# Kernel optimization log

Measured on AMD Instinct MI355X. Metric: run time of the kernel, lower is better.

## Reference

```python
import jax, jax.numpy as jnp
import numpy as np

NUM_IMUS = 13
NUM_PARAMS = 9
EPS = 1e-5
LN_EPS = 1e-5


def setup_inputs() -> dict:
    key = jax.random.key(0)
    k1, k2, k3 = jax.random.split(key, 3)
    d_model, S = 512, 2048
    hidden_states = jax.random.normal(k1, (1, S, d_model), dtype=jnp.float32)
    min_orig_accel_norm = jax.random.normal(k2, (1,), dtype=jnp.float32)
    W = jax.random.normal(k3, (d_model, NUM_IMUS * NUM_PARAMS), dtype=jnp.float32) * 0.02
    b = jnp.zeros((NUM_IMUS * NUM_PARAMS,), jnp.float32)
    ln_w = jnp.ones((d_model,), jnp.float32)
    ln_b = jnp.zeros((d_model,), jnp.float32)
    return {"hidden_states": hidden_states, "min_orig_accel_norm": min_orig_accel_norm,
            "ln_w": ln_w, "ln_b": ln_b, "W": W, "b": b}


def _layernorm(x, w, bias):
    mu = x.mean(-1, keepdims=True)
    var = ((x - mu) ** 2).mean(-1, keepdims=True)
    return (x - mu) * jax.lax.rsqrt(var + LN_EPS) * w + bias


def reference(hidden_states, min_orig_accel_norm, ln_w, ln_b, W, b):
    S = hidden_states.shape[1]
    x = _layernorm(hidden_states, ln_w, ln_b)
    # (1,S,117) -> (S, 9, 13); batch is always 1
    p = (x @ W + b).reshape(S, NUM_PARAMS, NUM_IMUS)
    c, c_th, phi, phi_th = p[:, 4], p[:, 5], p[:, 6], p[:, 7]  # (S,13) each
    d = jnp.sqrt(p[:, 1] ** 2 + EPS)                 # (S,13)
    k = d ** 2 / 4 + jax.nn.softplus(p[:, 0])
    d_th = jnp.sqrt(p[:, 3] ** 2 + EPS)
    k_th = d_th ** 2 / 4 + jax.nn.softplus(p[:, 2])
    noise_bias = p[:, 8].T                           # (13,S)
    om = jnp.sqrt(4 * k - d ** 2) / 2                # = sqrt(softplus(p0))
    om_th = jnp.sqrt(4 * k_th - d_th ** 2) / 2
    t = jnp.arange(S, dtype=jnp.float32)
    tstep = jnp.triu(t[None, :] - t[:, None])        # (S,S), entry (i,j)=j-i for j>=i
    ts = tstep[:, :, None]                           # (S,S,1)

    def src(a):  # params indexed by source step i, broadcast over target step j
        return a[:, None, :]                         # (S,1,13)

    lin = src(c) * jnp.exp(-src(d) / 2 * ts) * jnp.sin(ts * src(om) + src(phi))
    ang = src(c_th) * jnp.exp(-src(d_th) / 2 * ts) * jnp.sin(ts * src(om_th) + src(phi_th))
    mask = jnp.triu(jnp.ones((S, S), jnp.float32))[:, :, None]
    summed = ((lin + ang) * mask).sum(axis=0)        # (S,13): sum over source i<=j
    return summed.T + min_orig_accel_norm + noise_bias  # (13,S)
```

## Files before the change

### kernel.cpp

```cpp
#include <hip/hip_runtime.h>
#include <math.h>

#define S_LEN 2048
#define D_MODEL 512
#define NIMU 13
#define NCOL 117
#define CPAD 128
#define NKC 8
#define KCSTRIDE ((size_t)CPAD * S_LEN)

static __device__ __forceinline__ float softplus_f(float x) {
    return (x > 20.f) ? x : log1pf(expf(x));
}

static __device__ __forceinline__ void osc_init(float pk, float pd, float amp, float phi, float dtf,
                                                float& re, float& im, float& zr, float& zi)
{
    const float LOG2E = 1.4426950408889634f;
    const float INV2PI = 0.15915494309189535f;
    float d = sqrtf(pd * pd + 1e-5f);
    float kk = d * d * 0.25f + softplus_f(pk);
    float om = 0.5f * sqrtf(fmaxf(4.f * kk - d * d, 0.f));
    float y = -0.5f * d * LOG2E;
    float f = om * INV2PI;
    float ph = phi * INV2PI;
    float ez = __builtin_amdgcn_exp2f(y);
    zr = ez * __builtin_amdgcn_cosf(f);
    zi = ez * __builtin_amdgcn_sinf(f);
    float er = amp * __builtin_amdgcn_exp2f(dtf * y);
    float r = fmaf(dtf, f, ph); r -= floorf(r);
    re = er * __builtin_amdgcn_cosf(r);
    im = er * __builtin_amdgcn_sinf(r);
}

__global__ __launch_bounds__(256) void stats_kernel(const float* __restrict__ H,
                                                    float2* __restrict__ stats,
                                                    const float* __restrict__ W,
                                                    float* __restrict__ Wp,
                                                    float* __restrict__ out) {
    if (blockIdx.x < 104) out[blockIdx.x * 256 + threadIdx.x] = 0.f;
    if (threadIdx.x < CPAD) {
        int c = threadIdx.x;
        Wp[blockIdx.x * CPAD + c] = (c < NCOL) ? W[blockIdx.x * NCOL + c] : 0.f;
    }
    int wave = threadIdx.x >> 6;
    int lane = threadIdx.x & 63;
    int row = blockIdx.x * 4 + wave;
    const float* hr = H + row * D_MODEL;
    float4 a = *(const float4*)&hr[lane * 4];
    float4 b = *(const float4*)&hr[256 + lane * 4];
    float sum = a.x + a.y + a.z + a.w + b.x + b.y + b.z + b.w;
    #pragma unroll
    for (int off = 32; off; off >>= 1) sum += __shfl_down(sum, off);
    sum = __shfl(sum, 0);
    float mu = sum * (1.f / 512.f);
    float vs = 0.f;
    vs += (a.x - mu) * (a.x - mu); vs += (a.y - mu) * (a.y - mu);
    vs += (a.z - mu) * (a.z - mu); vs += (a.w - mu) * (a.w - mu);
    vs += (b.x - mu) * (b.x - mu); vs += (b.y - mu) * (b.y - mu);
    vs += (b.z - mu) * (b.z - mu); vs += (b.w - mu) * (b.w - mu);
    #pragma unroll
    for (int off = 32; off; off >>= 1) vs += __shfl_down(vs, off);
    if (lane == 0) {
        float var = vs * (1.f / 512.f);
        stats[row] = make_float2(mu, 1.0f / sqrtf(var + 1e-5f));
    }
}

__global__ __launch_bounds__(128) void proj_kernel(
    const float* __restrict__ H, const float2* __restrict__ stats,
    const float* __restrict__ lnw, const float* __restrict__ lnb,
    const float* __restrict__ Wp, float* __restrict__ Pt)
{
    __shared__ float Xt[64 * 32];
    __shared__ float Ws[64 * CPAD];
    int tid = threadIdx.x;
    int row0 = blockIdx.x * 32;
    int k0 = blockIdx.y * 64;

    {
        const float4* Wp4 = (const float4*)(Wp + k0 * CPAD);
        float4* Ws4 = (float4*)Ws;
        #pragma unroll
        for (int i = 0; i < 16; ++i) Ws4[tid + i * 128] = Wp4[tid + i * 128];
    }
    {
        int r = tid >> 2, fq = tid & 3;
        int row = row0 + r;
        float2 st = stats[row];
        const float4* H4 = (const float4*)(H + row * D_MODEL + k0);
        const float4* w4 = (const float4*)(lnw + k0);
        const float4* b4 = (const float4*)(lnb + k0);
        #pragma unroll
        for (int it = 0; it < 4; ++it) {
            int q = fq + it * 4;
            float4 h = H4[q], wv = w4[q], bv = b4[q];
            Xt[(4 * q + 0) * 32 + r] = (h.x - st.x) * st.y * wv.x + bv.x;
            Xt[(4 * q + 1) * 32 + r] = (h.y - st.x) * st.y * wv.y + bv.y;
            Xt[(4 * q + 2) * 32 + r] = (h.z - st.x) * st.y * wv.z + bv.z;
            Xt[(4 * q + 3) * 32 + r] = (h.w - st.x) * st.y * wv.w + bv.w;
        }
    }
    __syncthreads();

    int q8 = tid & 15;
    int rg = tid >> 4;
    float acc[4][8];
    #pragma unroll
    for (int a = 0; a < 4; ++a)
        for (int u = 0; u < 8; ++u) acc[a][u] = 0.f;

    #pragma unroll 4
    for (int k = 0; k < 64; ++k) {
        float4 xa = *(float4*)&Xt[k * 32 + 4 * rg];
        float4 w0 = *(float4*)&Ws[k * CPAD + 8 * q8];
        float4 w1 = *(float4*)&Ws[k * CPAD + 8 * q8 + 4];
        float xv[4] = {xa.x, xa.y, xa.z, xa.w};
        float wv[8] = {w0.x, w0.y, w0.z, w0.w, w1.x, w1.y, w1.z, w1.w};
        #pragma unroll
        for (int a = 0; a < 4; ++a)
            #pragma unroll
            for (int u = 0; u < 8; ++u)
                acc[a][u] = fmaf(xv[a], wv[u], acc[a][u]);
    }

    if (q8 < 15) {
        #pragma unroll
        for (int u = 0; u < 8; ++u) {
            int c = 8 * q8 + u;
            if (c < NCOL) {
                float4 v = make_float4(acc[0][u], acc[1][u], acc[2][u], acc[3][u]);
                *(float4*)&Pt[((size_t)blockIdx.y * CPAD + c) * S_LEN + row0 + 4 * rg] = v;
            }
        }
    }
}

__global__ __launch_bounds__(256) void reduce_kernel(const float* __restrict__ Pt,
                                                     const float* __restrict__ bias,
                                                     float* __restrict__ Pred)
{
    int c = blockIdx.y;
    int s4 = blockIdx.x * 256 + threadIdx.x;
    const float4* p4 = (const float4*)(Pt + (size_t)c * S_LEN) + s4;
    float b = bias[c];
    float4 acc = make_float4(b, b, b, b);
    #pragma unroll
    for (int kc = 0; kc < NKC; ++kc) {
        float4 v = p4[kc * (KCSTRIDE / 4)];
        acc.x += v.x; acc.y += v.y; acc.z += v.z; acc.w += v.w;
    }
    ((float4*)(Pred + (size_t)c * S_LEN))[s4] = acc;
}

__global__ __launch_bounds__(256) void main_kernel(
    const float* __restrict__ Pred,
    const float* __restrict__ minp, float* __restrict__ out)
{
    __shared__ float buf[4 * 128];
    int tid = threadIdx.x;
    int lane = tid & 63, w = tid >> 6;
    int m = blockIdx.y;
    int bx = blockIdx.x;

    int g = 0, base = 0;
    #pragma unroll 1
    for (;;) {
        int nb = (g + 4) >> 2;
        if (bx < base + nb) break;
        base += nb; ++g;
    }
    int sub = bx - base;
    int q = sub * 4 + w;

    float* accW = buf + w * 128;
    accW[lane] = 0.f; accW[lane + 64] = 0.f;
    __builtin_amdgcn_wave_barrier();

    if (q <= g) {
        int sc = q, tc = g - q;
        int i0 = sc * 64;
        float dtf = (float)(tc * 64);

        float pv[9];
        #pragma unroll
        for (int p = 0; p < 9; ++p)
            pv[p] = Pred[(size_t)(p * 13 + m) * S_LEN + i0 + lane];

        float reL, imL, zrL, ziL; osc_init(pv[0], pv[1], pv[4], pv[6], dtf, reL, imL, zrL, ziL);
        float reA, imA, zrA, ziA; osc_init(pv[2], pv[3], pv[5], pv[7], dtf, reA, imA, zrA, ziA);

        float a = 0.f;
        #pragma unroll 8
        for (int t = 0; t < 64; ++t) {
            a += imL + imA;
            accW[lane + t] = a;
            __builtin_amdgcn_wave_barrier();
            float nxt = accW[lane + t + 1];
            float tL = imL * ziL; float rL = fmaf(reL, zrL, -tL);
            imL = fmaf(reL, ziL, imL * zrL); reL = rL;
            float tA = imA * ziA; float rA = fmaf(reA, zrA, -tA);
            imA = fmaf(reA, ziA, imA * zrA); reA = rA;
            a = nxt;
        }
    }
    __syncthreads();

    if (tid < 128) {
        int j = g * 64 + tid;
        if (j < S_LEN) {
            float s = buf[tid] + buf[128 + tid] + buf[256 + tid] + buf[384 + tid];
            if (sub == 0 && tid < 64) {
                s += minp[0] + Pred[(size_t)(8 * 13 + m) * S_LEN + j];
            }
            atomicAdd(&out[m * S_LEN + j], s);
        }
    }
}

extern "C" void kernel_launch(void* const* d_in, const int* in_sizes, int n_in,
                              void* d_out, int out_size, void* d_ws, size_t ws_size,
                              hipStream_t stream)
{
    const float* H    = (const float*)d_in[0];
    const float* MINP = (const float*)d_in[1];
    const float* LNW  = (const float*)d_in[2];
    const float* LNB  = (const float*)d_in[3];
    const float* W    = (const float*)d_in[4];
    const float* B    = (const float*)d_in[5];
    float* out = (float*)d_out;

    const size_t PTSZ = (size_t)NKC * CPAD * S_LEN * sizeof(float);
    const size_t STSZ = S_LEN * sizeof(float2);
    const size_t WPSZ = (size_t)D_MODEL * CPAD * sizeof(float);

    char* ws = (char*)d_ws;
    float*  Pt    = (float*)ws;
    float2* stats = (float2*)(ws + PTSZ);
    float*  Wp    = (float*)(ws + PTSZ + STSZ);
    float*  Pred  = (float*)(ws + PTSZ + STSZ + WPSZ);

    stats_kernel<<<512, 256, 0, stream>>>(H, stats, W, Wp, out);
    proj_kernel<<<dim3(64, 8), 128, 0, stream>>>(H, stats, LNW, LNB, Wp, Pt);
    reduce_kernel<<<dim3(2, NCOL), 256, 0, stream>>>(Pt, B, Pred);
    main_kernel<<<dim3(144, NIMU), 256, 0, stream>>>(Pred, MINP, out);
}
```

Measured before the change: 92.04 us.

## Process two source steps per lane in main kernel to halve tile count

Each lane of the oscillator-sum kernel now handles two adjacent source steps, using 128-wide source chunks instead of 64. Both oscillators advance each step, and their contributions are interleaved through a 192-entry shared shift buffer per wave. This roughly halves the number of blocks (144 to 80 per IMU) and the per-step LDS shift traffic per source element, amortising the barrier and store/load costs. In exchange it uses more registers and a more complex indexing scheme with a wider 192-column output reduction.

After: 95.03 us. 1.03x slower.

```diff
diff --git a/kernel.cpp b/kernel.cpp
--- a/kernel.cpp
+++ b/kernel.cpp
@@ -157,7 +157,7 @@
     const float* __restrict__ Pred,
     const float* __restrict__ minp, float* __restrict__ out)
 {
-    __shared__ float buf[4 * 128];
+    __shared__ float buf[4 * 192];
     int tid = threadIdx.x;
     int lane = tid & 63, w = tid >> 6;
     int m = blockIdx.y;
@@ -166,50 +166,65 @@
     int g = 0, base = 0;
     #pragma unroll 1
     for (;;) {
-        int nb = (g + 4) >> 2;
+        int nb = ((g >> 1) + 4) >> 2;
         if (bx < base + nb) break;
         base += nb; ++g;
     }
     int sub = bx - base;
     int q = sub * 4 + w;
 
-    float* accW = buf + w * 128;
-    accW[lane] = 0.f; accW[lane + 64] = 0.f;
+    float* accW = buf + w * 192;
+    accW[lane] = 0.f; accW[lane + 64] = 0.f; accW[lane + 128] = 0.f;
     __builtin_amdgcn_wave_barrier();
 
-    if (q <= g) {
-        int sc = q, tc = g - q;
-        int i0 = sc * 64;
+    if (q <= (g >> 1)) {
+        int sc = q, tc = g - 2 * q;
+        int i0 = sc * 128;
         float dtf = (float)(tc * 64);
-
-        float pv[9];
-        #pragma unroll
-        for (int p = 0; p < 9; ++p)
-            pv[p] = Pred[(size_t)(p * 13 + m) * S_LEN + i0 + lane];
-
-        float reL, imL, zrL, ziL; osc_init(pv[0], pv[1], pv[4], pv[6], dtf, reL, imL, zrL, ziL);
-        float reA, imA, zrA, ziA; osc_init(pv[2], pv[3], pv[5], pv[7], dtf, reA, imA, zrA, ziA);
-
-        float a = 0.f;
+        int iA = i0 + 2 * lane;
+
+        float pvA[9], pvB[9];
+        #pragma unroll
+        for (int p = 0; p < 9; ++p) {
+            float2 v = *(const float2*)&Pred[(size_t)(p * 13 + m) * S_LEN + iA];
+            pvA[p] = v.x; pvB[p] = v.y;
+        }
+
+        float reLA, imLA, zrLA, ziLA; osc_init(pvA[0], pvA[1], pvA[4], pvA[6], dtf, reLA, imLA, zrLA, ziLA);
+        float reAA, imAA, zrAA, ziAA; osc_init(pvA[2], pvA[3], pvA[5], pvA[7], dtf, reAA, imAA, zrAA, ziAA);
+        float reLB, imLB, zrLB, ziLB; osc_init(pvB[0], pvB[1], pvB[4], pvB[6], dtf, reLB, imLB, zrLB, ziLB);
+        float reAB, imAB, zrAB, ziAB; osc_init(pvB[2], pvB[3], pvB[5], pvB[7], dtf, reAB, imAB, zrAB, ziAB);
+
+        float a0 = 0.f, a1 = 0.f;
+        float* wbase = accW + lane;
         #pragma unroll 8
         for (int t = 0; t < 64; ++t) {
-            a += imL + imA;
-            accW[lane + t] = a;
+            a0 += imLA + imAA;
+            a1 += imLB + imAB;
+            int c = (t >> 1) + (t & 1) * 96;
+            wbase[c] = a0;
             __builtin_amdgcn_wave_barrier();
-            float nxt = accW[lane + t + 1];
-            float tL = imL * ziL; float rL = fmaf(reL, zrL, -tL);
-            imL = fmaf(reL, ziL, imL * zrL); reL = rL;
-            float tA = imA * ziA; float rA = fmaf(reA, zrA, -tA);
-            imA = fmaf(reA, ziA, imA * zrA); reA = rA;
-            a = nxt;
-        }
+            float nxt = wbase[c + 1];
+            float tL = imLA * ziLA; float rL = fmaf(reLA, zrLA, -tL);
+            imLA = fmaf(reLA, ziLA, imLA * zrLA); reLA = rL;
+            float tA = imAA * ziAA; float rA = fmaf(reAA, zrAA, -tA);
+            imAA = fmaf(reAA, ziAA, imAA * zrAA); reAA = rA;
+            float tLB = imLB * ziLB; float rLB = fmaf(reLB, zrLB, -tLB);
+            imLB = fmaf(reLB, ziLB, imLB * zrLB); reLB = rLB;
+            float tAB = imAB * ziAB; float rAB = fmaf(reAB, zrAB, -tAB);
+            imAB = fmaf(reAB, ziAB, imAB * zrAB); reAB = rAB;
+            a0 = a1; a1 = nxt;
+        }
+        __builtin_amdgcn_wave_barrier();
+        wbase[32] = a0;
     }
     __syncthreads();
 
-    if (tid < 128) {
+    if (tid < 192) {
         int j = g * 64 + tid;
         if (j < S_LEN) {
-            float s = buf[tid] + buf[128 + tid] + buf[256 + tid] + buf[384 + tid];
+            int ad = (tid >> 1) + (tid & 1) * 96;
+            float s = buf[ad] + buf[192 + ad] + buf[384 + ad] + buf[576 + ad];
             if (sub == 0 && tid < 64) {
                 s += minp[0] + Pred[(size_t)(8 * 13 + m) * S_LEN + j];
             }
@@ -243,5 +258,5 @@
     stats_kernel<<<512, 256, 0, stream>>>(H, stats, W, Wp, out);
     proj_kernel<<<dim3(64, 8), 128, 0, stream>>>(H, stats, LNW, LNB, Wp, Pt);
     reduce_kernel<<<dim3(2, NCOL), 256, 0, stream>>>(Pt, B, Pred);
-    main_kernel<<<dim3(144, NIMU), 256, 0, stream>>>(Pred, MINP, out);
-}
+    main_kernel<<<dim3(80, NIMU), 256, 0, stream>>>(Pred, MINP, out);
+}
```
